# Kernel tuning notes

Measured on AMD Instinct MI355X. Metric: run time of the kernel, lower is better.

The kernel has to match this reference:

```python
import jax, jax.numpy as jnp
import numpy as np
from math import sqrt

N = 50000
E = 800000
D_EMB = 512
DK = 64
DV = 64
HEADS = 8


def setup_inputs() -> dict:
    key = jax.random.key(0)
    k1, k2, k3, k4 = jax.random.split(key, 4)
    x = jax.random.normal(k1, (N, D_EMB), dtype=jnp.float32)
    edge_index = jax.random.randint(k2, (2, E), 0, N, dtype=jnp.int64)
    out_qkv = (2 * DK + DV) * HEADS  # 1536
    W_qkv = jax.random.normal(k3, (out_qkv, D_EMB), dtype=jnp.float32) / sqrt(D_EMB)
    b_qkv = jnp.zeros((out_qkv,), dtype=jnp.float32)
    W_ff = jax.random.normal(k4, (D_EMB, DV * HEADS), dtype=jnp.float32) / sqrt(DV * HEADS)
    b_ff = jnp.zeros((D_EMB,), dtype=jnp.float32)
    return {"x": x, "edge_index": edge_index, "W_qkv": W_qkv, "b_qkv": b_qkv,
            "W_ff": W_ff, "b_ff": b_ff}


def _attention_message(Q, K, V, senders, receivers, n_nodes):
    # Q,K: [N, H, dK], V: [N, H, dV]; edge lists: [E]
    scale = 1.0 / sqrt(Q.shape[-1])
    # per-edge scores: [E, H]
    scores = jnp.einsum('ehd,ehd->eh', Q[receivers], K[senders]) * scale
    # segment softmax over incoming edges of each receiver
    smax = jax.ops.segment_max(scores, receivers, num_segments=n_nodes)  # [N, H]
    ex = jnp.exp(scores - smax[receivers])                               # [E, H]
    denom = jax.ops.segment_sum(ex, receivers, num_segments=n_nodes)    # [N, H]
    att = ex / denom[receivers]                                         # [E, H]
    # weighted scatter of V from senders to receivers: [N, H, dV]
    out = jax.ops.segment_sum(att[:, :, None] * V[senders], receivers,
                              num_segments=n_nodes)
    return out, att


def reference(x, edge_index, W_qkv, b_qkv, W_ff, b_ff):
    n_nodes = x.shape[0]
    qkv = x @ W_qkv.T + b_qkv  # [N, (2*dK+dV)*H]
    Q, K, V = jnp.split(qkv, [DK * HEADS, 2 * DK * HEADS], axis=-1)
    Q = Q.reshape(n_nodes, HEADS, DK)
    K = K.reshape(n_nodes, HEADS, DK)
    V = V.reshape(n_nodes, HEADS, DV)
    senders, receivers = edge_index[0], edge_index[1]
    msg, _ = _attention_message(Q, K, V, senders, receivers, n_nodes)
    # aggregate_heads: flatten heads and project to d_Embedding
    out = msg.reshape(n_nodes, HEADS * DV) @ W_ff.T + b_ff
    return out
```

## Files before the change

### kernel.cpp

```cpp
#include <hip/hip_runtime.h>

static constexpr int NN = 50000;
static constexpr int NE = 800000;
static constexpr int DEMB = 512;
static constexpr int QKV_OUT = 1536;

typedef _Float16 half8 __attribute__((ext_vector_type(8)));
typedef float floatx4 __attribute__((ext_vector_type(4)));

#define KQ_SCALE (127.0f / 5.5f)
#define KQ_DEQ   (5.5f / 127.0f)

static constexpr size_t OFF_QH   = 0;
static constexpr size_t OFF_K8   = 51200000;
static constexpr size_t OFF_V8   = 76800000;
static constexpr size_t OFF_MSG  = 102400000;
static constexpr size_t OFF_SRT  = 153600000;
static constexpr size_t OFF_DEG  = 156800000;
static constexpr size_t OFF_OFFA = 157000000;
static constexpr size_t OFF_CUR  = 157200064;
static constexpr size_t OFF_FLAG = 157400064;
static constexpr size_t OFF_WQH  = 157400128;
static constexpr size_t OFF_WFH  = 158972992;

typedef __attribute__((address_space(1))) const void* gas_ptr;
typedef __attribute__((address_space(3))) void* lds_ptr_t;

__device__ __forceinline__ void load_lds16(const void* g, void* l) {
  __builtin_amdgcn_global_load_lds((gas_ptr)g, (lds_ptr_t)l, 16, 0, 0);
}

__global__ __launch_bounds__(256)
void k_cvt(const float* __restrict__ in, _Float16* __restrict__ out, int n8) {
  int i = blockIdx.x * 256 + threadIdx.x;
  if (i < n8) {
    floatx4 a = *(const floatx4*)(in + (size_t)i * 8);
    floatx4 b = *(const floatx4*)(in + (size_t)i * 8 + 4);
    half8 h;
    #pragma unroll
    for (int q = 0; q < 4; ++q) { h[q] = (_Float16)a[q]; h[q + 4] = (_Float16)b[q]; }
    *(half8*)(out + (size_t)i * 8) = h;
  }
}

__global__ __launch_bounds__(64)
void k_detect64(const void* __restrict__ edge, int* __restrict__ flag) {
  if (threadIdx.x == 0) {
    const int* p = (const int*)edge;
    int is64 = 1;
    for (int i = 0; i < 16; ++i) if (p[2 * i + 1] != 0) is64 = 0;
    *flag = is64;
  }
}

__device__ __forceinline__ int edge_at(const void* edge, int row, int e, int is64) {
  if (is64) return (int)((const long long*)edge)[(size_t)row * NE + e];
  return ((const int*)edge)[(size_t)row * NE + e];
}

__global__ __launch_bounds__(256)
void k_histo(const void* __restrict__ edge, const int* __restrict__ flag,
             int* __restrict__ deg) {
  int e = blockIdx.x * 256 + threadIdx.x;
  if (e < NE) {
    int r = edge_at(edge, 1, e, *flag);
    atomicAdd(&deg[r], 1);
  }
}

__global__ __launch_bounds__(1024)
void k_scan(const int* __restrict__ deg, int* __restrict__ off,
            int* __restrict__ cur, int n) {
  __shared__ int sums[1024];
  int tid = threadIdx.x;
  int per = (n + 1023) >> 10;
  int start = tid * per;
  int end = start + per; if (end > n) end = n;
  int s = 0;
  for (int i = start; i < end; ++i) s += deg[i];
  sums[tid] = s;
  __syncthreads();
  for (int d = 1; d < 1024; d <<= 1) {
    int v = (tid >= d) ? sums[tid - d] : 0;
    __syncthreads();
    sums[tid] += v;
    __syncthreads();
  }
  int run = (tid == 0) ? 0 : sums[tid - 1];
  for (int i = start; i < end; ++i) {
    off[i] = run; cur[i] = run; run += deg[i];
  }
  if (tid == 0) off[n] = sums[1023];
}

__global__ __launch_bounds__(256)
void k_scatter(const void* __restrict__ edge, const int* __restrict__ flag,
               int* __restrict__ cur, int* __restrict__ srt) {
  int e = blockIdx.x * 256 + threadIdx.x;
  if (e < NE) {
    int is64 = *flag;
    int r = edge_at(edge, 1, e, is64);
    int s = edge_at(edge, 0, e, is64);
    int pos = atomicAdd(&cur[r], 1);
    srt[pos] = s;
  }
}

template<int MODE>
__global__ __launch_bounds__(256)
void k_gemm_nt(const _Float16* __restrict__ Ah, const _Float16* __restrict__ Bh,
               const float* __restrict__ bias,
               void* __restrict__ out0, void* __restrict__ out1, void* __restrict__ out2,
               int M, int N, int K) {
  __shared__ _Float16 As[128 * 32];
  __shared__ _Float16 Bs[128 * 32];
  const int tid = threadIdx.x;
  const int m0 = blockIdx.y * 128;
  const int n0 = blockIdx.x * 128;
  const int wid = tid >> 6, lane = tid & 63;
  const int wr = wid >> 1, wc = wid & 1;

  floatx4 acc[4][4];
  #pragma unroll
  for (int i = 0; i < 4; ++i)
    #pragma unroll
    for (int j = 0; j < 4; ++j)
      #pragma unroll
      for (int q = 0; q < 4; ++q) acc[i][j][q] = 0.f;

  const int srow = tid >> 2;
  const int sslot = tid & 3;
  const int fr = lane & 15;
  const int fslot = lane >> 4;

  int garow0 = m0 + srow;       if (garow0 >= M) garow0 = M - 1;
  int garow1 = m0 + srow + 64;  if (garow1 >= M) garow1 = M - 1;
  const int asl0 = sslot ^ ((srow >> 1) & 3);
  const int asl1 = sslot ^ (((srow + 64) >> 1) & 3);
  const int gbrow0 = n0 + srow, gbrow1 = n0 + srow + 64;

  for (int k0 = 0; k0 < K; k0 += 32) {
    load_lds16(Ah + (size_t)garow0 * K + k0 + asl0 * 8, (char*)As + wid * 1024);
    load_lds16(Ah + (size_t)garow1 * K + k0 + asl1 * 8, (char*)As + 4096 + wid * 1024);
    load_lds16(Bh + (size_t)gbrow0 * K + k0 + asl0 * 8, (char*)Bs + wid * 1024);
    load_lds16(Bh + (size_t)gbrow1 * K + k0 + asl1 * 8, (char*)Bs + 4096 + wid * 1024);
    __syncthreads();

    half8 a[4], b[4];
    #pragma unroll
    for (int m = 0; m < 4; ++m) {
      int R = wr * 64 + m * 16 + fr;
      a[m] = *(const half8*)(As + R * 32 + ((fslot ^ ((R >> 1) & 3)) << 3));
    }
    #pragma unroll
    for (int n = 0; n < 4; ++n) {
      int R = wc * 64 + n * 16 + fr;
      b[n] = *(const half8*)(Bs + R * 32 + ((fslot ^ ((R >> 1) & 3)) << 3));
    }
    #pragma unroll
    for (int m = 0; m < 4; ++m)
      #pragma unroll
      for (int n = 0; n < 4; ++n)
        acc[m][n] = __builtin_amdgcn_mfma_f32_16x16x32_f16(a[m], b[n], acc[m][n], 0, 0, 0);
    __syncthreads();
  }

  const int fq = (lane >> 4) << 2;
  #pragma unroll
  for (int m = 0; m < 4; ++m) {
    #pragma unroll
    for (int n = 0; n < 4; ++n) {
      int gn = n0 + wc * 64 + n * 16 + fr;
      float bv = bias[gn];
      #pragma unroll
      for (int q = 0; q < 4; ++q) {
        int gm = m0 + wr * 64 + m * 16 + fq + q;
        if (gm < M) {
          float val = acc[m][n][q] + bv;
          if (MODE == 0) {
            int region = gn >> 9;
            int col = gn & 511;
            size_t idx = (size_t)gm * 512 + col;
            if (region == 0) ((_Float16*)out0)[idx] = (_Float16)val;
            else {
              float s = fminf(fmaxf(val * KQ_SCALE, -127.f), 127.f);
              signed char c = (signed char)__float2int_rn(s);
              if (region == 1) ((signed char*)out1)[idx] = c;
              else             ((signed char*)out2)[idx] = c;
            }
          } else {
            ((float*)out0)[(size_t)gm * N + gn] = val;
          }
        }
      }
    }
  }
}

__global__ __launch_bounds__(256)
void k_attn(const _Float16* __restrict__ Qh, const signed char* __restrict__ K8,
            const signed char* __restrict__ V8, const int* __restrict__ off,
            const int* __restrict__ srt, _Float16* __restrict__ msg) {
  int r = blockIdx.x * 4 + (threadIdx.x >> 6);
  if (r >= NN) return;
  int lane = threadIdx.x & 63;
  int h = lane >> 3, j = lane & 7;
  int qoff = h * 64 + j * 8;

  half8 qh = *(const half8*)(Qh + (size_t)r * 512 + qoff);
  float q[8];
  #pragma unroll
  for (int i = 0; i < 8; ++i) q[i] = (float)qh[i] * 0.125f * KQ_DEQ;

  float denom = 0.f;
  float acc[8];
  #pragma unroll
  for (int i = 0; i < 8; ++i) acc[i] = 0.f;

  int e0 = off[r], e1 = off[r + 1];
  if (e1 <= e0) {
    half8 z = {};
    *(half8*)(msg + (size_t)r * 512 + qoff) = z;
    return;
  }

  auto gload = [&](uint2& k8, uint2& v8, int s) {
    k8 = *(const uint2*)(K8 + (size_t)s * 512 + qoff);
    v8 = *(const uint2*)(V8 + (size_t)s * 512 + qoff);
  };
  auto consume = [&](uint2 k8, uint2 v8) {
    int xw = (int)k8.x, yw = (int)k8.y;
    float p = 0.f;
    p += q[0] * (float)((xw << 24) >> 24);
    p += q[1] * (float)((xw << 16) >> 24);
    p += q[2] * (float)((xw << 8) >> 24);
    p += q[3] * (float)(xw >> 24);
    p += q[4] * (float)((yw << 24) >> 24);
    p += q[5] * (float)((yw << 16) >> 24);
    p += q[6] * (float)((yw << 8) >> 24);
    p += q[7] * (float)(yw >> 24);
    p += __shfl_xor(p, 1);
    p += __shfl_xor(p, 2);
    p += __shfl_xor(p, 4);
    float w = __expf(p);
    denom += w;
    int vx = (int)v8.x, vy = (int)v8.y;
    acc[0] += w * (float)((vx << 24) >> 24);
    acc[1] += w * (float)((vx << 16) >> 24);
    acc[2] += w * (float)((vx << 8) >> 24);
    acc[3] += w * (float)(vx >> 24);
    acc[4] += w * (float)((vy << 24) >> 24);
    acc[5] += w * (float)((vy << 16) >> 24);
    acc[6] += w * (float)((vy << 8) >> 24);
    acc[7] += w * (float)(vy >> 24);
  };
  auto sidx = [&](int e) { return srt[e < e1 ? e : e1 - 1]; };

  uint2 kb0, kb1, kb2, kb3, vb0, vb1, vb2, vb3;
  gload(kb0, vb0, sidx(e0));
  gload(kb1, vb1, sidx(e0 + 1));
  gload(kb2, vb2, sidx(e0 + 2));
  gload(kb3, vb3, sidx(e0 + 3));
  int sn0 = sidx(e0 + 4), sn1 = sidx(e0 + 5), sn2 = sidx(e0 + 6), sn3 = sidx(e0 + 7);

  int e = e0;
  for (; e + 4 <= e1; e += 4) {
    consume(kb0, vb0); gload(kb0, vb0, sn0);
    consume(kb1, vb1); gload(kb1, vb1, sn1);
    consume(kb2, vb2); gload(kb2, vb2, sn2);
    consume(kb3, vb3); gload(kb3, vb3, sn3);
    sn0 = sidx(e + 8); sn1 = sidx(e + 9); sn2 = sidx(e + 10); sn3 = sidx(e + 11);
  }
  int rem = e1 - e;
  if (rem > 0) consume(kb0, vb0);
  if (rem > 1) consume(kb1, vb1);
  if (rem > 2) consume(kb2, vb2);

  float inv = KQ_DEQ / denom;
  half8 oh;
  #pragma unroll
  for (int i = 0; i < 8; ++i) oh[i] = (_Float16)(acc[i] * inv);
  *(half8*)(msg + (size_t)r * 512 + qoff) = oh;
}

extern "C" void kernel_launch(void* const* d_in, const int* in_sizes, int n_in,
                              void* d_out, int out_size, void* d_ws, size_t ws_size,
                              hipStream_t stream) {
  const float* x     = (const float*)d_in[0];
  const void*  edge  = d_in[1];
  const float* W_qkv = (const float*)d_in[2];
  const float* b_qkv = (const float*)d_in[3];
  const float* W_ff  = (const float*)d_in[4];
  const float* b_ff  = (const float*)d_in[5];
  float* out = (float*)d_out;

  char* ws = (char*)d_ws;
  _Float16* Qh = (_Float16*)(ws + OFF_QH);
  signed char* K8 = (signed char*)(ws + OFF_K8);
  signed char* V8 = (signed char*)(ws + OFF_V8);
  _Float16* msgb = (_Float16*)(ws + OFF_MSG);
  _Float16* xh   = (_Float16*)(ws + OFF_MSG);
  int* srt  = (int*)(ws + OFF_SRT);
  int* deg  = (int*)(ws + OFF_DEG);
  int* offa = (int*)(ws + OFF_OFFA);
  int* cur  = (int*)(ws + OFF_CUR);
  int* flag = (int*)(ws + OFF_FLAG);
  _Float16* wqh = (_Float16*)(ws + OFF_WQH);
  _Float16* wfh = (_Float16*)(ws + OFF_WFH);

  hipMemsetAsync(deg, 0, NN * sizeof(int), stream);
  k_detect64<<<1, 64, 0, stream>>>(edge, flag);

  k_cvt<<<(NN * DEMB / 8 + 255) / 256, 256, 0, stream>>>(x, xh, NN * DEMB / 8);
  k_cvt<<<(QKV_OUT * DEMB / 8 + 255) / 256, 256, 0, stream>>>(W_qkv, wqh, QKV_OUT * DEMB / 8);
  k_cvt<<<(DEMB * DEMB / 8 + 255) / 256, 256, 0, stream>>>(W_ff, wfh, DEMB * DEMB / 8);

  k_gemm_nt<0><<<dim3(12, 391), 256, 0, stream>>>(
      xh, wqh, b_qkv, Qh, K8, V8, NN, QKV_OUT, DEMB);

  k_histo<<<(NE + 255) / 256, 256, 0, stream>>>(edge, flag, deg);
  k_scan<<<1, 1024, 0, stream>>>(deg, offa, cur, NN);
  k_scatter<<<(NE + 255) / 256, 256, 0, stream>>>(edge, flag, cur, srt);

  k_attn<<<(NN + 3) / 4, 256, 0, stream>>>(Qh, K8, V8, offa, srt, msgb);

  k_gemm_nt<1><<<dim3(4, 391), 256, 0, stream>>>(
      msgb, wfh, b_ff, out, nullptr, nullptr, NN, DEMB, DEMB);
}
```

Before: 598.0 us.

## Replace 128x128 GEMM with double-buffered 256x256 tile, 512-thread kernel

```diff
diff --git a/kernel.cpp b/kernel.cpp
--- a/kernel.cpp
+++ b/kernel.cpp
@@ -107,74 +107,101 @@
 }
 
 template<int MODE>
-__global__ __launch_bounds__(256)
-void k_gemm_nt(const _Float16* __restrict__ Ah, const _Float16* __restrict__ Bh,
+__global__ __launch_bounds__(512, 2)
+void k_gemm256(const _Float16* __restrict__ Ah, const _Float16* __restrict__ Bh,
                const float* __restrict__ bias,
                void* __restrict__ out0, void* __restrict__ out1, void* __restrict__ out2,
                int M, int N, int K) {
-  __shared__ _Float16 As[128 * 32];
-  __shared__ _Float16 Bs[128 * 32];
+  __shared__ _Float16 lds[2][2][256 * 64];
   const int tid = threadIdx.x;
-  const int m0 = blockIdx.y * 128;
-  const int n0 = blockIdx.x * 128;
+  const int m0 = blockIdx.y * 256;
+  const int n0 = blockIdx.x * 256;
   const int wid = tid >> 6, lane = tid & 63;
-  const int wr = wid >> 1, wc = wid & 1;
-
-  floatx4 acc[4][4];
-  #pragma unroll
-  for (int i = 0; i < 4; ++i)
-    #pragma unroll
-    for (int j = 0; j < 4; ++j)
-      #pragma unroll
-      for (int q = 0; q < 4; ++q) acc[i][j][q] = 0.f;
-
-  const int srow = tid >> 2;
-  const int sslot = tid & 3;
+  const int wr = wid >> 2, wc = wid & 3;
+
+  floatx4 acc[8][4];
+  #pragma unroll
+  for (int m = 0; m < 8; ++m)
+    #pragma unroll
+    for (int n = 0; n < 4; ++n)
+      #pragma unroll
+      for (int q = 0; q < 4; ++q) acc[m][n][q] = 0.f;
+
+  const int srow = tid >> 3;
+  const int sslot = tid & 7;
+  const int scg = sslot ^ (srow & 7);
+
+  int gar[4];
+  #pragma unroll
+  for (int c = 0; c < 4; ++c) {
+    int gr = m0 + srow + c * 64;
+    gar[c] = gr < M ? gr : M - 1;
+  }
+  const int gbr = n0 + srow;
+
   const int fr = lane & 15;
-  const int fslot = lane >> 4;
-
-  int garow0 = m0 + srow;       if (garow0 >= M) garow0 = M - 1;
-  int garow1 = m0 + srow + 64;  if (garow1 >= M) garow1 = M - 1;
-  const int asl0 = sslot ^ ((srow >> 1) & 3);
-  const int asl1 = sslot ^ (((srow + 64) >> 1) & 3);
-  const int gbrow0 = n0 + srow, gbrow1 = n0 + srow + 64;
-
-  for (int k0 = 0; k0 < K; k0 += 32) {
-    load_lds16(Ah + (size_t)garow0 * K + k0 + asl0 * 8, (char*)As + wid * 1024);
-    load_lds16(Ah + (size_t)garow1 * K + k0 + asl1 * 8, (char*)As + 4096 + wid * 1024);
-    load_lds16(Bh + (size_t)gbrow0 * K + k0 + asl0 * 8, (char*)Bs + wid * 1024);
-    load_lds16(Bh + (size_t)gbrow1 * K + k0 + asl1 * 8, (char*)Bs + 4096 + wid * 1024);
+  const int fs = lane >> 4;
+
+  const int KT = K >> 6;
+
+  {
+    _Float16* La = &lds[0][0][0];
+    _Float16* Lb = &lds[0][1][0];
+    #pragma unroll
+    for (int c = 0; c < 4; ++c) {
+      load_lds16(Ah + (size_t)gar[c] * K + scg * 8, (char*)La + c * 8192 + tid * 16);
+      load_lds16(Bh + (size_t)(gbr + c * 64) * K + scg * 8, (char*)Lb + c * 8192 + tid * 16);
+    }
+  }
+  __syncthreads();
+
+  for (int t = 0; t < KT; ++t) {
+    if (t + 1 < KT) {
+      int k0 = (t + 1) << 6;
+      _Float16* La = &lds[(t + 1) & 1][0][0];
+      _Float16* Lb = &lds[(t + 1) & 1][1][0];
+      #pragma unroll
+      for (int c = 0; c < 4; ++c) {
+        load_lds16(Ah + (size_t)gar[c] * K + k0 + scg * 8, (char*)La + c * 8192 + tid * 16);
+        load_lds16(Bh + (size_t)(gbr + c * 64) * K + k0 + scg * 8, (char*)Lb + c * 8192 + tid * 16);
+      }
+    }
+    const _Float16* La = &lds[t & 1][0][0];
+    const _Float16* Lb = &lds[t & 1][1][0];
+    #pragma unroll
+    for (int kk = 0; kk < 2; ++kk) {
+      half8 a[8], b[4];
+      #pragma unroll
+      for (int m = 0; m < 8; ++m) {
+        int R = wr * 128 + m * 16 + fr;
+        int s = (kk * 4 + fs) ^ (R & 7);
+        a[m] = *(const half8*)(La + R * 64 + s * 8);
+      }
+      #pragma unroll
+      for (int n = 0; n < 4; ++n) {
+        int R = wc * 64 + n * 16 + fr;
+        int s = (kk * 4 + fs) ^ (R & 7);
+        b[n] = *(const half8*)(Lb + R * 64 + s * 8);
+      }
+      #pragma unroll
+      for (int m = 0; m < 8; ++m)
+        #pragma unroll
+        for (int n = 0; n < 4; ++n)
+          acc[m][n] = __builtin_amdgcn_mfma_f32_16x16x32_f16(a[m], b[n], acc[m][n], 0, 0, 0);
+    }
     __syncthreads();
-
-    half8 a[4], b[4];
-    #pragma unroll
-    for (int m = 0; m < 4; ++m) {
-      int R = wr * 64 + m * 16 + fr;
-      a[m] = *(const half8*)(As + R * 32 + ((fslot ^ ((R >> 1) & 3)) << 3));
-    }
-    #pragma unroll
-    for (int n = 0; n < 4; ++n) {
-      int R = wc * 64 + n * 16 + fr;
-      b[n] = *(const half8*)(Bs + R * 32 + ((fslot ^ ((R >> 1) & 3)) << 3));
-    }
-    #pragma unroll
-    for (int m = 0; m < 4; ++m)
-      #pragma unroll
-      for (int n = 0; n < 4; ++n)
-        acc[m][n] = __builtin_amdgcn_mfma_f32_16x16x32_f16(a[m], b[n], acc[m][n], 0, 0, 0);
-    __syncthreads();
-  }
-
-  const int fq = (lane >> 4) << 2;
-  #pragma unroll
-  for (int m = 0; m < 4; ++m) {
+  }
+
+  const int fq = fs << 2;
+  #pragma unroll
+  for (int m = 0; m < 8; ++m) {
     #pragma unroll
     for (int n = 0; n < 4; ++n) {
       int gn = n0 + wc * 64 + n * 16 + fr;
       float bv = bias[gn];
       #pragma unroll
       for (int q = 0; q < 4; ++q) {
-        int gm = m0 + wr * 64 + m * 16 + fq + q;
+        int gm = m0 + wr * 128 + m * 16 + fq + q;
         if (gm < M) {
           float val = acc[m][n][q] + bv;
           if (MODE == 0) {
@@ -315,7 +342,7 @@
   k_cvt<<<(QKV_OUT * DEMB / 8 + 255) / 256, 256, 0, stream>>>(W_qkv, wqh, QKV_OUT * DEMB / 8);
   k_cvt<<<(DEMB * DEMB / 8 + 255) / 256, 256, 0, stream>>>(W_ff, wfh, DEMB * DEMB / 8);
 
-  k_gemm_nt<0><<<dim3(12, 391), 256, 0, stream>>>(
+  k_gemm256<0><<<dim3(6, 196), 512, 0, stream>>>(
       xh, wqh, b_qkv, Qh, K8, V8, NN, QKV_OUT, DEMB);
 
   k_histo<<<(NE + 255) / 256, 256, 0, stream>>>(edge, flag, deg);
@@ -324,6 +351,6 @@
 
   k_attn<<<(NN + 3) / 4, 256, 0, stream>>>(Qh, K8, V8, offa, srt, msgb);
 
-  k_gemm_nt<1><<<dim3(4, 391), 256, 0, stream>>>(
+  k_gemm256<1><<<dim3(2, 196), 512, 0, stream>>>(
       msgb, wfh, b_ff, out, nullptr, nullptr, NN, DEMB, DEMB);
 }
```

Measured after the change: 568.3 us. 5.0% less time.
